# Kernel tuning notes

Measured on AMD Instinct MI355X. Metric: run time of the kernel, lower is better.

## Reference

```python
import jax, jax.numpy as jnp
import numpy as np

ATTEN_SIZE = 5  # half-window; module-global atten_size in source (0 there is non-functional)
B, S, D_IN, HID, OUT = 8, 2048, 512, 512, 2


def _xavier(key, shape):
    fan_in, fan_out = shape
    std = (2.0 / (fan_in + fan_out)) ** 0.5
    return jax.random.normal(key, shape, dtype=jnp.float32) * std


def setup_inputs() -> dict:
    key = jax.random.key(0)
    ks = jax.random.split(key, 8)
    return {
        "x": jax.random.normal(ks[0], (B, S, D_IN), dtype=jnp.float32),
        "W1": _xavier(ks[1], (D_IN, HID)),
        "b1": jnp.zeros((1, 1, HID), dtype=jnp.float32),
        "Wq": _xavier(ks[2], (HID, HID)),
        "Wk": _xavier(ks[3], (HID, HID)),
        "Wv": _xavier(ks[4], (HID, HID)),
        "W2": _xavier(ks[5], (HID, HID)),
        "b2": jnp.zeros((1, 1, HID), dtype=jnp.float32),
        "Wfc": _xavier(ks[6], (HID, OUT)),
        "bfc": jnp.zeros((OUT,), dtype=jnp.float32),
    }


def reference(x, W1, b1, Wq, Wk, Wv, W2, b2, Wfc, bfc):
    A = ATTEN_SIZE
    Wn = 2 * A + 1
    h = jax.nn.relu(x @ W1 + b1)                      # [B,S,H]
    b, s, hd = h.shape
    padded = jnp.pad(h, ((0, 0), (A, A), (0, 0)))     # [B,S+2A,H]
    # torch pad+roll(k)+stack+slice equals reversed window: x_nei[p, j] = padded[p + 2A - j]
    idx = jnp.arange(s)[:, None] + (2 * A - jnp.arange(Wn))[None, :]  # [S,Wn]
    x_nei = padded[:, idx, :]                         # [B,S,Wn,H]
    q = h @ Wq                                        # [B,S,H]
    k = x_nei @ Wk                                    # [B,S,Wn,H]
    v = x_nei @ Wv                                    # [B,S,Wn,H]
    scale = jnp.asarray(np.sqrt(float(hd)), dtype=h.dtype)
    scores = jnp.einsum('bsh,bswh->bsw', q, k)[:, :, None, :] / scale  # [B,S,1,Wn]
    # Faithful to torch.nn.Softmax(dim=2) on a singleton dim -> all ones
    w = jax.nn.softmax(scores, axis=2)                # [B,S,1,Wn]
    aw = jnp.einsum('bsjw,bswh->bsjh', w, v).reshape(b, s, hd)  # [B,S,H]
    out = jax.nn.relu(aw @ W2 + b2) @ Wfc + bfc       # [B,S,OUT]
    return out, aw
```

## Files before the change

### kernel.cpp

```cpp
#include <hip/hip_runtime.h>
#include <stdint.h>

#define B_   8
#define S_   2048
#define HID_ 512
#define M_   (B_ * S_)
#define AW_  5

typedef __attribute__((ext_vector_type(8))) short bf16x8;
typedef __attribute__((ext_vector_type(4))) float f32x4;
typedef unsigned short u16;

__device__ __forceinline__ u16 f2bf(float f) {
    uint32_t u = __builtin_bit_cast(uint32_t, f);
    u += 0x7FFFu + ((u >> 16) & 1u);
    return (u16)(u >> 16);
}
__device__ __forceinline__ float bf2f(u16 h) {
    uint32_t u = ((uint32_t)h) << 16;
    return __builtin_bit_cast(float, u);
}

__device__ __forceinline__ void gload16(const void* g, void* l) {
    __builtin_amdgcn_global_load_lds(
        (const __attribute__((address_space(1))) void*)(uintptr_t)g,
        (__attribute__((address_space(3))) void*)(uint32_t)(uintptr_t)l,
        16, 0, 0);
}

#define WAITV(n)  asm volatile("s_waitcnt vmcnt(" #n ")" ::: "memory")
#define WAITLG0() asm volatile("s_waitcnt lgkmcnt(0)" ::: "memory")

__global__ __launch_bounds__(256) void prep_w(const float* __restrict__ W1,
                                              const float* __restrict__ Wv,
                                              const float* __restrict__ W2,
                                              u16* __restrict__ W1t,
                                              u16* __restrict__ Wvt,
                                              u16* __restrict__ W2t,
                                              int do_w2) {
    const int wsel = blockIdx.x >> 8;
    if (wsel == 2 && !do_w2) return;
    const float* src = wsel == 0 ? W1 : (wsel == 1 ? Wv : W2);
    u16* dst = wsel == 0 ? W1t : (wsel == 1 ? Wvt : W2t);
    const int t  = blockIdx.x & 255;
    const int n0 = (t & 15) * 32, k0 = (t >> 4) * 32;
    __shared__ float tile[32][33];
    const int tr = threadIdx.x >> 5, tc = threadIdx.x & 31;
#pragma unroll
    for (int p = 0; p < 4; ++p)
        tile[tr + p * 8][tc] = src[(long)(k0 + tr + p * 8) * HID_ + n0 + tc];
    __syncthreads();
#pragma unroll
    for (int p = 0; p < 4; ++p)
        dst[(long)(n0 + tr + p * 8) * HID_ + k0 + tc] = f2bf(tile[tc][tr + p * 8]);
}

__global__ __launch_bounds__(256) void trans_w2(const float* __restrict__ W2,
                                                u16* __restrict__ W2t) {
    __shared__ float tile[32][33];
    const int k0 = blockIdx.y * 32, n0 = blockIdx.x * 32;
    const int tr = threadIdx.x >> 5, tc = threadIdx.x & 31;
#pragma unroll
    for (int p = 0; p < 4; ++p)
        tile[tr + p * 8][tc] = W2[(long)(k0 + tr + p * 8) * HID_ + n0 + tc];
    __syncthreads();
#pragma unroll
    for (int p = 0; p < 4; ++p)
        W2t[(long)(n0 + tr + p * 8) * HID_ + k0 + tc] = f2bf(tile[tc][tr + p * 8]);
}

__global__ __launch_bounds__(256, 2) void gemm1_f32a(const float* __restrict__ A,
                                                     const u16* __restrict__ Bt,
                                                     const float* __restrict__ bias,
                                                     u16* __restrict__ C) {
    __shared__ __attribute__((aligned(16))) u16 As[2][128 * 64];
    __shared__ __attribute__((aligned(16))) u16 Bs[2][128 * 64];

    const int tid = threadIdx.x;
    const int bid = blockIdx.x;
    const int swz = (bid & 7) * 64 + (bid >> 3);
    const int  bn   = (swz & 3) * 128;
    const long brow = (long)(swz >> 2) * 128;

    const int w  = tid >> 6;
    const int l  = tid & 63;
    const int wm = (w >> 1) * 64;
    const int wn = (w & 1) * 64;
    const int lr  = l & 15;
    const int lkb = (l >> 4) * 16;
    const int sw  = (lr & 7) << 4;

    const int r0 = tid >> 2;
    const int c0 = (tid & 3) * 16;
    const int r1 = 64 + r0;
    const float* ga0 = A + (brow + r0) * 512 + c0;
    const float* ga1 = A + (brow + r1) * 512 + c0;
    char* lw = (char*)&As[0][0];
    const int wb00 = r0 * 128 + ((c0 * 2 +  0) ^ ((r0 & 7) << 4));
    const int wb01 = r0 * 128 + ((c0 * 2 + 16) ^ ((r0 & 7) << 4));
    const int wb10 = r1 * 128 + ((c0 * 2 +  0) ^ ((r1 & 7) << 4));
    const int wb11 = r1 * 128 + ((c0 * 2 + 16) ^ ((r1 & 7) << 4));

    int pq[4];
    const u16* srcB[4];
#pragma unroll
    for (int q = 0; q < 4; ++q) {
        const int p   = tid * 16 + q * 4096;
        const int row = p >> 7;
        const int cb  = (p & 127) ^ ((row & 7) << 4);
        pq[q]   = p;
        srcB[q] = Bt + (long)(bn + row) * 512 + (cb >> 1);
    }

    f32x4 acc[4][4];
#pragma unroll
    for (int i = 0; i < 4; ++i)
#pragma unroll
        for (int j = 0; j < 4; ++j) {
            f32x4 z = {0.f, 0.f, 0.f, 0.f};
            acc[i][j] = z;
        }

    float4 ra[4], rb[4];

#define LOADA(k0)                                                        \
    {                                                                    \
        _Pragma("unroll") for (int u = 0; u < 4; ++u) {                  \
            ra[u] = *(const float4*)(ga0 + (k0) + u * 4);                \
            rb[u] = *(const float4*)(ga1 + (k0) + u * 4);                \
        }                                                                \
    }
#define CVTWRITE(buf)                                                    \
    {                                                                    \
        union { u16 u[8]; int4 v; } q0, q1, q2, q3;                      \
        q0.u[0]=f2bf(ra[0].x); q0.u[1]=f2bf(ra[0].y); q0.u[2]=f2bf(ra[0].z); q0.u[3]=f2bf(ra[0].w); \
        q0.u[4]=f2bf(ra[1].x); q0.u[5]=f2bf(ra[1].y); q0.u[6]=f2bf(ra[1].z); q0.u[7]=f2bf(ra[1].w); \
        q1.u[0]=f2bf(ra[2].x); q1.u[1]=f2bf(ra[2].y); q1.u[2]=f2bf(ra[2].z); q1.u[3]=f2bf(ra[2].w); \
        q1.u[4]=f2bf(ra[3].x); q1.u[5]=f2bf(ra[3].y); q1.u[6]=f2bf(ra[3].z); q1.u[7]=f2bf(ra[3].w); \
        q2.u[0]=f2bf(rb[0].x); q2.u[1]=f2bf(rb[0].y); q2.u[2]=f2bf(rb[0].z); q2.u[3]=f2bf(rb[0].w); \
        q2.u[4]=f2bf(rb[1].x); q2.u[5]=f2bf(rb[1].y); q2.u[6]=f2bf(rb[1].z); q2.u[7]=f2bf(rb[1].w); \
        q3.u[0]=f2bf(rb[2].x); q3.u[1]=f2bf(rb[2].y); q3.u[2]=f2bf(rb[2].z); q3.u[3]=f2bf(rb[2].w); \
        q3.u[4]=f2bf(rb[3].x); q3.u[5]=f2bf(rb[3].y); q3.u[6]=f2bf(rb[3].z); q3.u[7]=f2bf(rb[3].w); \
        *(int4*)(lw + (buf) * 16384 + wb00) = q0.v;                      \
        *(int4*)(lw + (buf) * 16384 + wb01) = q1.v;                      \
        *(int4*)(lw + (buf) * 16384 + wb10) = q2.v;                      \
        *(int4*)(lw + (buf) * 16384 + wb11) = q3.v;                      \
    }
#define STAGEB(buf, k0)                                                  \
    {                                                                    \
        _Pragma("unroll") for (int q = 0; q < 4; ++q)                    \
            gload16(srcB[q] + (k0), (char*)&Bs[buf][0] + pq[q]);         \
    }

    LOADA(0);
    STAGEB(0, 0);
    CVTWRITE(0);
    __syncthreads();

    int cur = 0;
    for (int t = 0; t < 8; ++t) {
        if (t < 7) {
            LOADA((t + 1) * 64);
            STAGEB(cur ^ 1, (t + 1) * 64);
        }
#pragma unroll
        for (int kk = 0; kk < 2; ++kk) {
            bf16x8 af[4], bfr[4];
#pragma unroll
            for (int i = 0; i < 4; ++i) {
                const int off = (wm + i * 16 + lr) * 128 + ((kk * 64 + lkb) ^ sw);
                af[i] = *(const bf16x8*)((const char*)&As[cur][0] + off);
            }
#pragma unroll
            for (int j = 0; j < 4; ++j) {
                const int off = (wn + j * 16 + lr) * 128 + ((kk * 64 + lkb) ^ sw);
                bfr[j] = *(const bf16x8*)((const char*)&Bs[cur][0] + off);
            }
#pragma unroll
            for (int i = 0; i < 4; ++i)
#pragma unroll
                for (int j = 0; j < 4; ++j)
                    acc[i][j] = __builtin_amdgcn_mfma_f32_16x16x32_bf16(
                        af[i], bfr[j], acc[i][j], 0, 0, 0);
        }
        if (t < 7) CVTWRITE(cur ^ 1);
        __syncthreads();
        cur ^= 1;
    }
#undef LOADA
#undef CVTWRITE
#undef STAGEB

    float bv[4];
#pragma unroll
    for (int j = 0; j < 4; ++j) bv[j] = bias[bn + wn + j * 16 + lr];
    const int rq = (l >> 4) * 4;
#pragma unroll
    for (int i = 0; i < 4; ++i)
#pragma unroll
        for (int q = 0; q < 4; ++q) {
            const long row = brow + wm + i * 16 + rq + q;
            u16* crow = C + row * 512 + bn + wn + lr;
#pragma unroll
            for (int j = 0; j < 4; ++j)
                crow[j * 16] = f2bf(fmaxf(acc[i][j][q] + bv[j], 0.f));
        }
}

template <int EPI>
__global__ __launch_bounds__(256, 2) void gemm_pipe(const u16* __restrict__ A,
                                                    const u16* __restrict__ Bt,
                                                    const float* __restrict__ b2,
                                                    const float* __restrict__ Wfc,
                                                    u16* __restrict__ C,
                                                    float* __restrict__ partials) {
    __shared__ __attribute__((aligned(16))) u16 As[3][64 * 64];
    __shared__ __attribute__((aligned(16))) u16 Bs[3][128 * 64];

    const int tid = threadIdx.x;
    const int bid = blockIdx.x;
    const int swz = (bid & 7) * 128 + (bid >> 3);
    const int  bn   = (swz & 3) * 128;
    const long brow = (long)(swz >> 2) * 64;

    const int w  = tid >> 6;
    const int l  = tid & 63;
    const int wn = w * 32;
    const int lr  = l & 15;
    const int lkb = (l >> 4) * 16;
    const int sw  = (lr & 7) << 4;

    int pa[2], pb[4];
    const u16* srcA[2];
    const u16* srcB[4];
#pragma unroll
    for (int q = 0; q < 2; ++q) {
        const int p   = tid * 16 + q * 4096;
        const int row = p >> 7;
        const int cb  = (p & 127) ^ ((row & 7) << 4);
        pa[q]   = p;
        srcA[q] = A + (brow + row) * 512 + (cb >> 1);
    }
#pragma unroll
    for (int q = 0; q < 4; ++q) {
        const int p   = tid * 16 + q * 4096;
        const int row = p >> 7;
        const int cb  = (p & 127) ^ ((row & 7) << 4);
        pb[q]   = p;
        srcB[q] = Bt + (long)(bn + row) * 512 + (cb >> 1);
    }

    f32x4 acc[4][2];
#pragma unroll
    for (int i = 0; i < 4; ++i)
#pragma unroll
        for (int j = 0; j < 2; ++j) {
            f32x4 z = {0.f, 0.f, 0.f, 0.f};
            acc[i][j] = z;
        }

#define STAGEP(buf, k0)                                                  \
    {                                                                    \
        gload16(srcA[0] + (k0), (char*)&As[buf][0] + pa[0]);             \
        gload16(srcA[1] + (k0), (char*)&As[buf][0] + pa[1]);             \
        gload16(srcB[0] + (k0), (char*)&Bs[buf][0] + pb[0]);             \
        gload16(srcB[1] + (k0), (char*)&Bs[buf][0] + pb[1]);             \
        gload16(srcB[2] + (k0), (char*)&Bs[buf][0] + pb[2]);             \
        gload16(srcB[3] + (k0), (char*)&Bs[buf][0] + pb[3]);             \
    }

    STAGEP(0, 0);
    STAGEP(1, 64);
    WAITV(6);
    __builtin_amdgcn_s_barrier();

#pragma unroll
    for (int t = 0; t < 8; ++t) {
        if (t < 6) {
            const int nb = (t + 2) % 3;
            if (nb == 0)      STAGEP(0, (t + 2) * 64)
            else if (nb == 1) STAGEP(1, (t + 2) * 64)
            else              STAGEP(2, (t + 2) * 64)
        }

        const int cb = t % 3;
        const char* ab = cb == 0 ? (const char*)&As[0][0]
                       : cb == 1 ? (const char*)&As[1][0] : (const char*)&As[2][0];
        const char* bb = cb == 0 ? (const char*)&Bs[0][0]
                       : cb == 1 ? (const char*)&Bs[1][0] : (const char*)&Bs[2][0];
#pragma unroll
        for (int kk = 0; kk < 2; ++kk) {
            bf16x8 af[4], bfr[2];
#pragma unroll
            for (int i = 0; i < 4; ++i) {
                const int off = (i * 16 + lr) * 128 + ((kk * 64 + lkb) ^ sw);
                af[i] = *(const bf16x8*)(ab + off);
            }
#pragma unroll
            for (int j = 0; j < 2; ++j) {
                const int off = (wn + j * 16 + lr) * 128 + ((kk * 64 + lkb) ^ sw);
                bfr[j] = *(const bf16x8*)(bb + off);
            }
#pragma unroll
            for (int i = 0; i < 4; ++i)
#pragma unroll
                for (int j = 0; j < 2; ++j)
                    acc[i][j] = __builtin_amdgcn_mfma_f32_16x16x32_bf16(
                        af[i], bfr[j], acc[i][j], 0, 0, 0);
        }

        if (t < 7) {
            WAITLG0();
            __builtin_amdgcn_sched_barrier(0);
            if (t < 6) WAITV(6);
            else       WAITV(0);
            __builtin_amdgcn_s_barrier();
        }
    }
#undef STAGEP

    const int rq = (l >> 4) * 4;
    if (EPI == 0) {
#pragma unroll
        for (int i = 0; i < 4; ++i)
#pragma unroll
            for (int q = 0; q < 4; ++q) {
                const long row = brow + i * 16 + rq + q;
                u16* crow = C + row * 512 + bn + wn + lr;
#pragma unroll
                for (int j = 0; j < 2; ++j)
                    crow[j * 16] = f2bf(acc[i][j][q]);
            }
    } else {
        float bvv[2], w0v[2], w1v[2];
#pragma unroll
        for (int j = 0; j < 2; ++j) {
            const int col = bn + wn + j * 16 + lr;
            bvv[j] = b2[col];
            w0v[j] = Wfc[2 * col];
            w1v[j] = Wfc[2 * col + 1];
        }
        const int slot = (bn >> 7) * 4 + w;
#pragma unroll
        for (int i = 0; i < 4; ++i)
#pragma unroll
            for (int q = 0; q < 4; ++q) {
                float s0 = 0.f, s1 = 0.f;
#pragma unroll
                for (int j = 0; j < 2; ++j) {
                    const float v = fmaxf(acc[i][j][q] + bvv[j], 0.f);
                    s0 += v * w0v[j];
                    s1 += v * w1v[j];
                }
#pragma unroll
                for (int m = 1; m < 16; m <<= 1) {
                    s0 += __shfl_xor(s0, m);
                    s1 += __shfl_xor(s1, m);
                }
                if (lr == 0) {
                    const long row = brow + i * 16 + rq + q;
                    float* pp = partials + ((long)slot * M_ + row) * 2;
                    pp[0] = s0;
                    pp[1] = s1;
                }
            }
    }
}

__global__ __launch_bounds__(256) void winsum_f(const u16* __restrict__ g,
                                                u16* __restrict__ awb,
                                                float* __restrict__ awf) {
    const long idx = (long)blockIdx.x * 256 + threadIdx.x;
    const int  c8  = (int)(idx & 63);
    const long bs  = idx >> 6;
    const int  s   = (int)(bs & (S_ - 1));

    float acc[8] = {};
#pragma unroll
    for (int d = -AW_; d <= AW_; ++d) {
        const int ss = s + d;
        if (0 <= ss && ss < S_) {
            const int4 v = *(const int4*)&g[(bs + d) * HID_ + c8 * 8];
            const u16* u = (const u16*)&v;
#pragma unroll
            for (int e = 0; e < 8; ++e) acc[e] += bf2f(u[e]);
        }
    }
    union { u16 u[8]; int4 v; } r;
#pragma unroll
    for (int e = 0; e < 8; ++e) r.u[e] = f2bf(acc[e]);
    *(int4*)&awb[bs * HID_ + c8 * 8] = r.v;
    float4 o0 = {acc[0], acc[1], acc[2], acc[3]};
    float4 o1 = {acc[4], acc[5], acc[6], acc[7]};
    *(float4*)&awf[bs * HID_ + c8 * 8]     = o0;
    *(float4*)&awf[bs * HID_ + c8 * 8 + 4] = o1;
}

__global__ __launch_bounds__(256) void fc_reduce(const float* __restrict__ partials,
                                                 const float* __restrict__ bfc,
                                                 float* __restrict__ out) {
    const int row = blockIdx.x * 256 + threadIdx.x;
    float s0 = bfc[0], s1 = bfc[1];
#pragma unroll
    for (int p = 0; p < 16; ++p) {
        s0 += partials[((long)p * M_ + row) * 2 + 0];
        s1 += partials[((long)p * M_ + row) * 2 + 1];
    }
    out[row * 2 + 0] = s0;
    out[row * 2 + 1] = s1;
}

extern "C" void kernel_launch(void* const* d_in, const int* in_sizes, int n_in,
                              void* d_out, int out_size, void* d_ws, size_t ws_size,
                              hipStream_t stream) {
    const float* x   = (const float*)d_in[0];
    const float* W1  = (const float*)d_in[1];
    const float* b1  = (const float*)d_in[2];
    const float* Wv  = (const float*)d_in[5];
    const float* W2  = (const float*)d_in[6];
    const float* b2  = (const float*)d_in[7];
    const float* Wfc = (const float*)d_in[8];
    const float* bfc = (const float*)d_in[9];

    float* out_part = (float*)d_out;
    float* aw_f32   = (float*)d_out + (long)M_ * 2;

    unsigned char* ws = (unsigned char*)d_ws;

    u16* W1t = (u16*)aw_f32;
    u16* Wvt = W1t + 262144;

    u16* h   = (u16*)ws;
    u16* g   = (u16*)ws + 8388608;
    u16* awb = h;
    float* partials = (float*)(ws + (17l << 20));

    const bool big = ws_size >= ((size_t)34 << 20);
    u16* W2t = big ? (u16*)(ws + (33l << 20)) : g;

    prep_w<<<768, 256, 0, stream>>>(W1, Wv, W2, W1t, Wvt, W2t, big ? 1 : 0);
    gemm1_f32a<<<512, 256, 0, stream>>>(x, W1t, b1, h);
    gemm_pipe<0><<<1024, 256, 0, stream>>>(h, Wvt, nullptr, nullptr, g, nullptr);
    winsum_f<<<4096, 256, 0, stream>>>(g, awb, aw_f32);
    if (!big)
        trans_w2<<<dim3(16, 16), 256, 0, stream>>>(W2, W2t);
    gemm_pipe<1><<<1024, 256, 0, stream>>>(awb, W2t, b2, Wfc, nullptr, partials);
    fc_reduce<<<64, 256, 0, stream>>>(partials, bfc, out_part);
}
```

Before: 83.97 us.

## Enlarge GEMM tile to 256x128 with 512-thread blocks and MFMA priority

Replaces the 64x128 tile GEMM with a 256x128 tile run by 8 waves (2x4 layout), each wave computing 128x32. This raises reuse of the B tile and cuts the number of blocks from 1024 to 256. It also wraps the MFMA section in s_setprio to favour compute issue. The trade-offs are that 256 blocks on a large GPU may underfill the CUs, and the larger LDS footprint (about 144KB for triple buffering) likely limits occupancy to one block per CU.

```diff
diff --git a/kernel.cpp b/kernel.cpp
--- a/kernel.cpp
+++ b/kernel.cpp
@@ -208,69 +208,70 @@
 }
 
 template <int EPI>
-__global__ __launch_bounds__(256, 2) void gemm_pipe(const u16* __restrict__ A,
-                                                    const u16* __restrict__ Bt,
-                                                    const float* __restrict__ b2,
-                                                    const float* __restrict__ Wfc,
-                                                    u16* __restrict__ C,
-                                                    float* __restrict__ partials) {
-    __shared__ __attribute__((aligned(16))) u16 As[3][64 * 64];
+__global__ __launch_bounds__(512, 2) void gemm256(const u16* __restrict__ A,
+                                                  const u16* __restrict__ Bt,
+                                                  const float* __restrict__ b2,
+                                                  const float* __restrict__ Wfc,
+                                                  u16* __restrict__ C,
+                                                  float* __restrict__ partials) {
+    __shared__ __attribute__((aligned(16))) u16 As[3][256 * 64];
     __shared__ __attribute__((aligned(16))) u16 Bs[3][128 * 64];
 
     const int tid = threadIdx.x;
     const int bid = blockIdx.x;
-    const int swz = (bid & 7) * 128 + (bid >> 3);
+    const int swz = (bid & 7) * 32 + (bid >> 3);
     const int  bn   = (swz & 3) * 128;
-    const long brow = (long)(swz >> 2) * 64;
+    const long brow = (long)(swz >> 2) * 256;
 
     const int w  = tid >> 6;
     const int l  = tid & 63;
-    const int wn = w * 32;
+    const int wm = (w >> 2) * 128;
+    const int wn = (w & 3) * 32;
     const int lr  = l & 15;
     const int lkb = (l >> 4) * 16;
     const int sw  = (lr & 7) << 4;
 
-    int pa[2], pb[4];
-    const u16* srcA[2];
-    const u16* srcB[4];
-#pragma unroll
-    for (int q = 0; q < 2; ++q) {
-        const int p   = tid * 16 + q * 4096;
+    int pa[4], pb[2];
+    const u16* srcA[4];
+    const u16* srcB[2];
+#pragma unroll
+    for (int q = 0; q < 4; ++q) {
+        const int p   = tid * 16 + q * 8192;
         const int row = p >> 7;
         const int cb  = (p & 127) ^ ((row & 7) << 4);
         pa[q]   = p;
         srcA[q] = A + (brow + row) * 512 + (cb >> 1);
     }
 #pragma unroll
-    for (int q = 0; q < 4; ++q) {
-        const int p   = tid * 16 + q * 4096;
+    for (int q = 0; q < 2; ++q) {
+        const int p   = tid * 16 + q * 8192;
         const int row = p >> 7;
         const int cb  = (p & 127) ^ ((row & 7) << 4);
         pb[q]   = p;
         srcB[q] = Bt + (long)(bn + row) * 512 + (cb >> 1);
     }
 
-    f32x4 acc[4][2];
-#pragma unroll
-    for (int i = 0; i < 4; ++i)
+    f32x4 acc[8][2];
+#pragma unroll
+    for (int i = 0; i < 8; ++i)
 #pragma unroll
         for (int j = 0; j < 2; ++j) {
             f32x4 z = {0.f, 0.f, 0.f, 0.f};
             acc[i][j] = z;
         }
 
-#define STAGEP(buf, k0)                                                  \
+#define STG(buf, k0)                                                     \
     {                                                                    \
         gload16(srcA[0] + (k0), (char*)&As[buf][0] + pa[0]);             \
         gload16(srcA[1] + (k0), (char*)&As[buf][0] + pa[1]);             \
+        gload16(srcA[2] + (k0), (char*)&As[buf][0] + pa[2]);             \
+        gload16(srcA[3] + (k0), (char*)&As[buf][0] + pa[3]);             \
         gload16(srcB[0] + (k0), (char*)&Bs[buf][0] + pb[0]);             \
         gload16(srcB[1] + (k0), (char*)&Bs[buf][0] + pb[1]);             \
-        gload16(srcB[2] + (k0), (char*)&Bs[buf][0] + pb[2]);             \
-        gload16(srcB[3] + (k0), (char*)&Bs[buf][0] + pb[3]);             \
-    }
-
-    STAGEP(0, 0);
-    STAGEP(1, 64);
+    }
+
+    STG(0, 0);
+    STG(1, 64);
     WAITV(6);
     __builtin_amdgcn_s_barrier();
 
@@ -278,36 +279,39 @@
     for (int t = 0; t < 8; ++t) {
         if (t < 6) {
             const int nb = (t + 2) % 3;
-            if (nb == 0)      STAGEP(0, (t + 2) * 64)
-            else if (nb == 1) STAGEP(1, (t + 2) * 64)
-            else              STAGEP(2, (t + 2) * 64)
-        }
-
-        const int cb = t % 3;
-        const char* ab = cb == 0 ? (const char*)&As[0][0]
-                       : cb == 1 ? (const char*)&As[1][0] : (const char*)&As[2][0];
-        const char* bb = cb == 0 ? (const char*)&Bs[0][0]
-                       : cb == 1 ? (const char*)&Bs[1][0] : (const char*)&Bs[2][0];
+            if (nb == 0)      STG(0, (t + 2) * 64)
+            else if (nb == 1) STG(1, (t + 2) * 64)
+            else              STG(2, (t + 2) * 64)
+        }
+
+        const int cbuf = t % 3;
+        const char* ab = cbuf == 0 ? (const char*)&As[0][0]
+                       : cbuf == 1 ? (const char*)&As[1][0] : (const char*)&As[2][0];
+        const char* bb = cbuf == 0 ? (const char*)&Bs[0][0]
+                       : cbuf == 1 ? (const char*)&Bs[1][0] : (const char*)&Bs[2][0];
+
+        __builtin_amdgcn_s_setprio(1);
 #pragma unroll
         for (int kk = 0; kk < 2; ++kk) {
-            bf16x8 af[4], bfr[2];
-#pragma unroll
-            for (int i = 0; i < 4; ++i) {
-                const int off = (i * 16 + lr) * 128 + ((kk * 64 + lkb) ^ sw);
-                af[i] = *(const bf16x8*)(ab + off);
-            }
+            bf16x8 af[8], bfr[2];
 #pragma unroll
             for (int j = 0; j < 2; ++j) {
                 const int off = (wn + j * 16 + lr) * 128 + ((kk * 64 + lkb) ^ sw);
                 bfr[j] = *(const bf16x8*)(bb + off);
             }
 #pragma unroll
-            for (int i = 0; i < 4; ++i)
+            for (int i = 0; i < 8; ++i) {
+                const int off = (wm + i * 16 + lr) * 128 + ((kk * 64 + lkb) ^ sw);
+                af[i] = *(const bf16x8*)(ab + off);
+            }
+#pragma unroll
+            for (int i = 0; i < 8; ++i)
 #pragma unroll
                 for (int j = 0; j < 2; ++j)
                     acc[i][j] = __builtin_amdgcn_mfma_f32_16x16x32_bf16(
                         af[i], bfr[j], acc[i][j], 0, 0, 0);
         }
+        __builtin_amdgcn_s_setprio(0);
 
         if (t < 7) {
             WAITLG0();
@@ -317,15 +321,15 @@
             __builtin_amdgcn_s_barrier();
         }
     }
-#undef STAGEP
+#undef STG
 
     const int rq = (l >> 4) * 4;
     if (EPI == 0) {
 #pragma unroll
-        for (int i = 0; i < 4; ++i)
+        for (int i = 0; i < 8; ++i)
 #pragma unroll
             for (int q = 0; q < 4; ++q) {
-                const long row = brow + i * 16 + rq + q;
+                const long row = brow + wm + i * 16 + rq + q;
                 u16* crow = C + row * 512 + bn + wn + lr;
 #pragma unroll
                 for (int j = 0; j < 2; ++j)
@@ -340,9 +344,9 @@
             w0v[j] = Wfc[2 * col];
             w1v[j] = Wfc[2 * col + 1];
         }
-        const int slot = (bn >> 7) * 4 + w;
-#pragma unroll
-        for (int i = 0; i < 4; ++i)
+        const int slot = (bn >> 7) * 4 + (w & 3);
+#pragma unroll
+        for (int i = 0; i < 8; ++i)
 #pragma unroll
             for (int q = 0; q < 4; ++q) {
                 float s0 = 0.f, s1 = 0.f;
@@ -358,7 +362,7 @@
                     s1 += __shfl_xor(s1, m);
                 }
                 if (lr == 0) {
-                    const long row = brow + i * 16 + rq + q;
+                    const long row = brow + wm + i * 16 + rq + q;
                     float* pp = partials + ((long)slot * M_ + row) * 2;
                     pp[0] = s0;
                     pp[1] = s1;
@@ -440,10 +444,10 @@
 
     prep_w<<<768, 256, 0, stream>>>(W1, Wv, W2, W1t, Wvt, W2t, big ? 1 : 0);
     gemm1_f32a<<<512, 256, 0, stream>>>(x, W1t, b1, h);
-    gemm_pipe<0><<<1024, 256, 0, stream>>>(h, Wvt, nullptr, nullptr, g, nullptr);
+    gemm256<0><<<256, 512, 0, stream>>>(h, Wvt, nullptr, nullptr, g, nullptr);
     winsum_f<<<4096, 256, 0, stream>>>(g, awb, aw_f32);
     if (!big)
         trans_w2<<<dim3(16, 16), 256, 0, stream>>>(W2, W2t);
-    gemm_pipe<1><<<1024, 256, 0, stream>>>(awb, W2t, b2, Wfc, nullptr, partials);
+    gemm256<1><<<256, 512, 0, stream>>>(awb, W2t, b2, Wfc, nullptr, partials);
     fc_reduce<<<64, 256, 0, stream>>>(partials, bfc, out_part);
 }
```

Result: faster. 79.76 us (-5.0%).
